# Optimization experiments

Measured on AMD Instinct MI355X. Metric: run time of the kernel, lower is better.

Reference implementation:

```python
import jax, jax.numpy as jnp
import numpy as np
import math

B, N, D, H, K = 8, 256, 128, 256, 128


def setup_inputs() -> dict:
    key = jax.random.key(0)
    ks = jax.random.split(key, 8)
    # forward args
    x = jax.random.uniform(ks[0], (B, N, N), dtype=jnp.float32) * 3.0  # pairwise distances
    atom_embeds = jax.random.normal(ks[1], (B, N, D), dtype=jnp.float32)
    # params of nn.Linear(2D, H) and nn.Linear(H, 2) (store as [in, out])
    lim1 = 1.0 / math.sqrt(2 * D)
    W1 = jax.random.uniform(ks[2], (2 * D, H), minval=-lim1, maxval=lim1, dtype=jnp.float32)
    b1 = jax.random.uniform(ks[3], (H,), minval=-lim1, maxval=lim1, dtype=jnp.float32)
    lim2 = 1.0 / math.sqrt(H)
    W2 = jax.random.uniform(ks[4], (H, 2), minval=-lim2, maxval=lim2, dtype=jnp.float32)
    b2 = jax.random.uniform(ks[5], (2,), minval=-lim2, maxval=lim2, dtype=jnp.float32)
    # RBF params: means ~ U(0,3), temps ~ U(0.1,10)
    means = jax.random.uniform(ks[6], (K,), minval=0.0, maxval=3.0, dtype=jnp.float32)
    temps = jax.random.uniform(ks[7], (K,), minval=0.1, maxval=10.0, dtype=jnp.float32)
    return {"x": x, "atom_embeds": atom_embeds, "W1": W1, "b1": b1,
            "W2": W2, "b2": b2, "means": means, "temps": temps}


def reference(x, atom_embeds, W1, b1, W2, b2, means, temps):
    d = atom_embeds.shape[-1]
    scale = 1.0 / math.sqrt(2 * d)
    # Split-weight trick: cat([e_i, e_j]) @ W1 == e_i @ W1[:D] + e_j @ W1[D:]
    # (same math, avoids materializing the [B,N,N,2D] concat)
    hi = jnp.einsum('bnd,dh->bnh', atom_embeds, W1[:d])   # [B,N,H]
    hj = jnp.einsum('bnd,dh->bnh', atom_embeds, W1[d:])   # [B,N,H]
    h = jax.nn.relu(hi[:, :, None, :] + hj[:, None, :, :] + b1)  # [B,N,N,H]
    edge_features = (jnp.einsum('bijh,ho->bijo', h, W2) + b2) * scale  # [B,N,N,2]
    mul = edge_features[..., 0:1]   # [B,N,N,1]
    bias = edge_features[..., 1:2]  # [B,N,N,1]
    v = mul * x[..., None] + bias   # [B,N,N,1]
    temp = jnp.abs(temps)
    # RBF gaussian basis expansion -> [B,N,N,K]
    return jnp.exp(-jnp.square(v - means) * temp)
```

## Files before the change

kernel.cpp:

```cpp
#include <hip/hip_runtime.h>
#include <hip/hip_bf16.h>


#define NB 8
#define NN 256
#define ND 128
#define NH 256
#define NK 128
#define GI 2

typedef float f32x4 __attribute__((ext_vector_type(4)));

__global__ __launch_bounds__(256) void precompute_hij(
    const float* __restrict__ atom, const float* __restrict__ W1,
    const float* __restrict__ b1,
    float* __restrict__ hi, float* __restrict__ hjbT) {
  const int h = threadIdx.x;
  const int base = blockIdx.x * 8;
  const int b  = base >> 8;
  const int j0 = base & 255;
  __shared__ float a[8][ND];
  for (int t = threadIdx.x; t < 8 * ND; t += 256) {
    a[t >> 7][t & 127] = atom[(size_t)base * ND + t];
  }
  __syncthreads();
  float acc0[8], acc1[8];
  const float bv = b1[h];
#pragma unroll
  for (int r = 0; r < 8; ++r) { acc0[r] = 0.f; acc1[r] = bv; }
  for (int d = 0; d < ND; ++d) {
    const float w0 = W1[d * NH + h];
    const float w1 = W1[(ND + d) * NH + h];
#pragma unroll
    for (int r = 0; r < 8; ++r) {
      acc0[r] = fmaf(a[r][d], w0, acc0[r]);
      acc1[r] = fmaf(a[r][d], w1, acc1[r]);
    }
  }
#pragma unroll
  for (int r = 0; r < 8; ++r) {
    hi[(size_t)(base + r) * NH + h] = acc0[r];
    hjbT[((size_t)b * NH + h) * NN + (j0 + r)] = acc1[r];
  }
}

__global__ __launch_bounds__(256) void compute_v(
    const float* __restrict__ x,
    const float* __restrict__ hi, const float* __restrict__ hjbT,
    const float* __restrict__ W2, const float* __restrict__ b2,
    float* __restrict__ v) {
  const int b    = blockIdx.x & 7;
  const int i0   = (blockIdx.x >> 3) * GI;
  const int lane = threadIdx.x & 63;
  const int wave = threadIdx.x >> 6;

  __shared__ float part0[4][GI][NN];
  __shared__ float part1[4][GI][NN];

  const float* __restrict__ hjrow  = hjbT + ((size_t)b * NH + wave * 64) * NN;
  const float* __restrict__ w2row  = W2 + wave * 128;
  const float* __restrict__ hibase = hi + ((size_t)(b * NN + i0)) * NH + wave * 64;

  float acc0[GI][4], acc1[GI][4];
#pragma unroll
  for (int r = 0; r < GI; ++r)
#pragma unroll
    for (int q = 0; q < 4; ++q) { acc0[r][q] = 0.f; acc1[r][q] = 0.f; }

#pragma unroll 8
  for (int hh = 0; hh < 64; ++hh) {
    const float4 hj4 = *reinterpret_cast<const float4*>(hjrow + (size_t)hh * NN + 4 * lane);
    const float w0 = w2row[2 * hh];
    const float w1 = w2row[2 * hh + 1];
#pragma unroll
    for (int r = 0; r < GI; ++r) {
      const float hih = hibase[(size_t)r * NH + hh];
      const float a0 = fmaxf(hih + hj4.x, 0.f);
      const float a1 = fmaxf(hih + hj4.y, 0.f);
      const float a2 = fmaxf(hih + hj4.z, 0.f);
      const float a3 = fmaxf(hih + hj4.w, 0.f);
      acc0[r][0] = fmaf(a0, w0, acc0[r][0]); acc1[r][0] = fmaf(a0, w1, acc1[r][0]);
      acc0[r][1] = fmaf(a1, w0, acc0[r][1]); acc1[r][1] = fmaf(a1, w1, acc1[r][1]);
      acc0[r][2] = fmaf(a2, w0, acc0[r][2]); acc1[r][2] = fmaf(a2, w1, acc1[r][2]);
      acc0[r][3] = fmaf(a3, w0, acc0[r][3]); acc1[r][3] = fmaf(a3, w1, acc1[r][3]);
    }
  }
#pragma unroll
  for (int r = 0; r < GI; ++r) {
    *reinterpret_cast<float4*>(&part0[wave][r][4 * lane]) =
        make_float4(acc0[r][0], acc0[r][1], acc0[r][2], acc0[r][3]);
    *reinterpret_cast<float4*>(&part1[wave][r][4 * lane]) =
        make_float4(acc1[r][0], acc1[r][1], acc1[r][2], acc1[r][3]);
  }
  __syncthreads();

  {
    const int t = threadIdx.x;
    const float scale = 0.0625f;
    const float b20 = b2[0], b21 = b2[1];
#pragma unroll
    for (int r = 0; r < GI; ++r) {
      const float s0 = part0[0][r][t] + part0[1][r][t] + part0[2][r][t] + part0[3][r][t];
      const float s1 = part1[0][r][t] + part1[1][r][t] + part1[2][r][t] + part1[3][r][t];
      const float mul  = (s0 + b20) * scale;
      const float bias = (s1 + b21) * scale;
      const size_t bij = (size_t)(b * NN + i0 + r) * NN + t;
      v[bij] = fmaf(mul, x[bij], bias);
    }
  }
}

__global__ __launch_bounds__(256) void rbf_store(
    const float* __restrict__ v,
    const float* __restrict__ means, const float* __restrict__ temps,
    float* __restrict__ out) {
  const int idx = blockIdx.x * 256 + threadIdx.x;
  const int k0  = (idx & 31) * 4;

  const float LOG2E = 1.44269504088896340736f;
  const float4 mv = *reinterpret_cast<const float4*>(means + k0);
  float4 tv = *reinterpret_cast<const float4*>(temps + k0);
  const float t0 = -fabsf(tv.x) * LOG2E;
  const float t1 = -fabsf(tv.y) * LOG2E;
  const float t2 = -fabsf(tv.z) * LOG2E;
  const float t3 = -fabsf(tv.w) * LOG2E;

  const float* __restrict__ vp = v + (idx >> 5);
  float* __restrict__ op = out + (size_t)idx * 4;

#pragma unroll 4
  for (int s = 0; s < 32; ++s) {
    const float vj = vp[s * 16384];
    const float d0 = vj - mv.x;
    const float d1 = vj - mv.y;
    const float d2 = vj - mv.z;
    const float d3 = vj - mv.w;
    f32x4 e;
    e.x = __builtin_amdgcn_exp2f(d0 * d0 * t0);
    e.y = __builtin_amdgcn_exp2f(d1 * d1 * t1);
    e.z = __builtin_amdgcn_exp2f(d2 * d2 * t2);
    e.w = __builtin_amdgcn_exp2f(d3 * d3 * t3);
    *reinterpret_cast<f32x4*>(op + (size_t)s * 2097152) = e;
  }
}

extern "C" void kernel_launch(void* const* d_in, const int* in_sizes, int n_in,
                              void* d_out, int out_size, void* d_ws, size_t ws_size,
                              hipStream_t stream) {
  const float* x     = (const float*)d_in[0];
  const float* atom  = (const float*)d_in[1];
  const float* W1    = (const float*)d_in[2];
  const float* b1    = (const float*)d_in[3];
  const float* W2    = (const float*)d_in[4];
  const float* b2    = (const float*)d_in[5];
  const float* means = (const float*)d_in[6];
  const float* temps = (const float*)d_in[7];
  float* out = (float*)d_out;

  float* hi   = (float*)d_ws;
  float* hjbT = hi + (size_t)NB * NN * NH;
  float* v    = hjbT + (size_t)NB * NH * NN;

  precompute_hij<<<NB * NN / 8, 256, 0, stream>>>(atom, W1, b1, hi, hjbT);
  compute_v<<<NB * NN / GI, 256, 0, stream>>>(x, hi, hjbT, W2, b2, v);
  rbf_store<<<2048, 256, 0, stream>>>(v, means, temps, out);
}
```

Before: 84.93 us.

## Fuse edge MLP and RBF expansion into one kernel with register-resident hj

Merges the compute_v and rbf_store kernels into a single edge_rbf kernel, so the intermediate v array never goes through global memory and one launch is dropped. Each block caches a 64-column hj slice in registers and loops over 8 rows i. Per row it reduces the four wave partial sums through double-buffered shared memory, then broadcasts v with shuffles to compute and store the RBF outputs. This removes v traffic and a launch, but it adds a barrier per row and heavy register pressure from the 64-float hj array, which may lower occupancy for the store-bound output phase.

Measured after the change: 79.17 us. 6.8% less time.

```diff
diff --git a/kernel.cpp b/kernel.cpp
--- a/kernel.cpp
+++ b/kernel.cpp
@@ -7,9 +7,11 @@
 #define ND 128
 #define NH 256
 #define NK 128
-#define GI 2
+#define IG 8
+#define JT 64
 
 typedef float f32x4 __attribute__((ext_vector_type(4)));
+typedef float f32x2 __attribute__((ext_vector_type(2)));
 
 __global__ __launch_bounds__(256) void precompute_hij(
     const float* __restrict__ atom, const float* __restrict__ W1,
@@ -44,103 +46,85 @@
   }
 }
 
-__global__ __launch_bounds__(256) void compute_v(
+__global__ __launch_bounds__(256) void edge_rbf(
     const float* __restrict__ x,
     const float* __restrict__ hi, const float* __restrict__ hjbT,
     const float* __restrict__ W2, const float* __restrict__ b2,
-    float* __restrict__ v) {
-  const int b    = blockIdx.x & 7;
-  const int i0   = (blockIdx.x >> 3) * GI;
-  const int lane = threadIdx.x & 63;
-  const int wave = threadIdx.x >> 6;
-
-  __shared__ float part0[4][GI][NN];
-  __shared__ float part1[4][GI][NN];
-
-  const float* __restrict__ hjrow  = hjbT + ((size_t)b * NH + wave * 64) * NN;
-  const float* __restrict__ w2row  = W2 + wave * 128;
-  const float* __restrict__ hibase = hi + ((size_t)(b * NN + i0)) * NH + wave * 64;
-
-  float acc0[GI][4], acc1[GI][4];
-#pragma unroll
-  for (int r = 0; r < GI; ++r)
-#pragma unroll
-    for (int q = 0; q < 4; ++q) { acc0[r][q] = 0.f; acc1[r][q] = 0.f; }
-
-#pragma unroll 8
-  for (int hh = 0; hh < 64; ++hh) {
-    const float4 hj4 = *reinterpret_cast<const float4*>(hjrow + (size_t)hh * NN + 4 * lane);
-    const float w0 = w2row[2 * hh];
-    const float w1 = w2row[2 * hh + 1];
-#pragma unroll
-    for (int r = 0; r < GI; ++r) {
-      const float hih = hibase[(size_t)r * NH + hh];
-      const float a0 = fmaxf(hih + hj4.x, 0.f);
-      const float a1 = fmaxf(hih + hj4.y, 0.f);
-      const float a2 = fmaxf(hih + hj4.z, 0.f);
-      const float a3 = fmaxf(hih + hj4.w, 0.f);
-      acc0[r][0] = fmaf(a0, w0, acc0[r][0]); acc1[r][0] = fmaf(a0, w1, acc1[r][0]);
-      acc0[r][1] = fmaf(a1, w0, acc0[r][1]); acc1[r][1] = fmaf(a1, w1, acc1[r][1]);
-      acc0[r][2] = fmaf(a2, w0, acc0[r][2]); acc1[r][2] = fmaf(a2, w1, acc1[r][2]);
-      acc0[r][3] = fmaf(a3, w0, acc0[r][3]); acc1[r][3] = fmaf(a3, w1, acc1[r][3]);
-    }
-  }
-#pragma unroll
-  for (int r = 0; r < GI; ++r) {
-    *reinterpret_cast<float4*>(&part0[wave][r][4 * lane]) =
-        make_float4(acc0[r][0], acc0[r][1], acc0[r][2], acc0[r][3]);
-    *reinterpret_cast<float4*>(&part1[wave][r][4 * lane]) =
-        make_float4(acc1[r][0], acc1[r][1], acc1[r][2], acc1[r][3]);
-  }
-  __syncthreads();
-
-  {
-    const int t = threadIdx.x;
-    const float scale = 0.0625f;
-    const float b20 = b2[0], b21 = b2[1];
-#pragma unroll
-    for (int r = 0; r < GI; ++r) {
-      const float s0 = part0[0][r][t] + part0[1][r][t] + part0[2][r][t] + part0[3][r][t];
-      const float s1 = part1[0][r][t] + part1[1][r][t] + part1[2][r][t] + part1[3][r][t];
-      const float mul  = (s0 + b20) * scale;
-      const float bias = (s1 + b21) * scale;
-      const size_t bij = (size_t)(b * NN + i0 + r) * NN + t;
-      v[bij] = fmaf(mul, x[bij], bias);
-    }
-  }
-}
-
-__global__ __launch_bounds__(256) void rbf_store(
-    const float* __restrict__ v,
     const float* __restrict__ means, const float* __restrict__ temps,
     float* __restrict__ out) {
-  const int idx = blockIdx.x * 256 + threadIdx.x;
-  const int k0  = (idx & 31) * 4;
+  const int b  = blockIdx.x & 7;
+  const int jt = (blockIdx.x >> 3) & 3;
+  const int ig = blockIdx.x >> 5;
+  const int i0 = ig * IG;
+  const int j0 = jt * JT;
+  const int lane = threadIdx.x & 63;
+  const int wv = __builtin_amdgcn_readfirstlane((int)(threadIdx.x >> 6));
+  const int h0 = wv * 64;
 
+  __shared__ f32x2 part[2][4][64];
+
+  float hj[64];
+  {
+    const float* __restrict__ hjb = hjbT + ((size_t)b * NH + h0) * NN + j0 + lane;
+#pragma unroll
+    for (int hh = 0; hh < 64; ++hh) hj[hh] = hjb[(size_t)hh * NN];
+  }
+
+  const float* __restrict__ w2s = W2 + 2 * h0;
+  const float* hib  = hi + ((size_t)(b * NN + i0)) * NH + h0;
+  const float* xrow = x + ((size_t)(b * NN + i0)) * NN + j0;
+
+  const float scale = 0.0625f;
+  const float b20 = b2[0], b21 = b2[1];
+
+  const int k0 = (threadIdx.x & 31) * 4;
+  const int jj = threadIdx.x >> 5;
   const float LOG2E = 1.44269504088896340736f;
-  const float4 mv = *reinterpret_cast<const float4*>(means + k0);
-  float4 tv = *reinterpret_cast<const float4*>(temps + k0);
+  const f32x4 mv = *reinterpret_cast<const f32x4*>(means + k0);
+  const f32x4 tv = *reinterpret_cast<const f32x4*>(temps + k0);
   const float t0 = -fabsf(tv.x) * LOG2E;
   const float t1 = -fabsf(tv.y) * LOG2E;
   const float t2 = -fabsf(tv.z) * LOG2E;
   const float t3 = -fabsf(tv.w) * LOG2E;
 
-  const float* __restrict__ vp = v + (idx >> 5);
-  float* __restrict__ op = out + (size_t)idx * 4;
+  float* outb = out + (((size_t)(b * NN + i0)) * NN + j0) * NK + k0;
 
-#pragma unroll 4
-  for (int s = 0; s < 32; ++s) {
-    const float vj = vp[s * 16384];
-    const float d0 = vj - mv.x;
-    const float d1 = vj - mv.y;
-    const float d2 = vj - mv.z;
-    const float d3 = vj - mv.w;
-    f32x4 e;
-    e.x = __builtin_amdgcn_exp2f(d0 * d0 * t0);
-    e.y = __builtin_amdgcn_exp2f(d1 * d1 * t1);
-    e.z = __builtin_amdgcn_exp2f(d2 * d2 * t2);
-    e.w = __builtin_amdgcn_exp2f(d3 * d3 * t3);
-    *reinterpret_cast<f32x4*>(op + (size_t)s * 2097152) = e;
+  for (int i = 0; i < IG; ++i) {
+    float s0 = 0.f, s1 = 0.f;
+#pragma unroll
+    for (int hh = 0; hh < 64; ++hh) {
+      const float a = fmaxf(hib[hh] + hj[hh], 0.f);
+      s0 = fmaf(a, w2s[2 * hh],     s0);
+      s1 = fmaf(a, w2s[2 * hh + 1], s1);
+    }
+    part[i & 1][wv][lane] = f32x2{s0, s1};
+    __syncthreads();
+
+    const f32x2 p0 = part[i & 1][0][lane];
+    const f32x2 p1 = part[i & 1][1][lane];
+    const f32x2 p2 = part[i & 1][2][lane];
+    const f32x2 p3 = part[i & 1][3][lane];
+    const float mul  = ((p0.x + p1.x + p2.x + p3.x) + b20) * scale;
+    const float bias = ((p0.y + p1.y + p2.y + p3.y) + b21) * scale;
+    const float vv = fmaf(mul, xrow[lane], bias);
+
+    float* __restrict__ oi = outb + (size_t)i * NN * NK;
+#pragma unroll
+    for (int p = 0; p < 8; ++p) {
+      const float vj = __shfl(vv, jj + 8 * p, 64);
+      const float d0 = vj - mv.x;
+      const float d1 = vj - mv.y;
+      const float d2 = vj - mv.z;
+      const float d3 = vj - mv.w;
+      f32x4 e;
+      e.x = __builtin_amdgcn_exp2f(d0 * d0 * t0);
+      e.y = __builtin_amdgcn_exp2f(d1 * d1 * t1);
+      e.z = __builtin_amdgcn_exp2f(d2 * d2 * t2);
+      e.w = __builtin_amdgcn_exp2f(d3 * d3 * t3);
+      *reinterpret_cast<f32x4*>(oi + (size_t)(jj + 8 * p) * NK) = e;
+    }
+    hib  += NH;
+    xrow += NN;
   }
 }
 
@@ -159,9 +143,7 @@
 
   float* hi   = (float*)d_ws;
   float* hjbT = hi + (size_t)NB * NN * NH;
-  float* v    = hjbT + (size_t)NB * NH * NN;
 
   precompute_hij<<<NB * NN / 8, 256, 0, stream>>>(atom, W1, b1, hi, hjbT);
-  compute_v<<<NB * NN / GI, 256, 0, stream>>>(x, hi, hjbT, W2, b2, v);
-  rbf_store<<<2048, 256, 0, stream>>>(v, means, temps, out);
+  edge_rbf<<<NB * (NN / JT) * (NN / IG), 256, 0, stream>>>(x, hi, hjbT, W2, b2, means, temps, out);
 }
```
